# Optimization experiments

Measured on AMD Instinct MI355X. Metric: run time of the kernel, lower is better.

The kernel has to match this reference:

```python
import jax, jax.numpy as jnp
import numpy as np

N = 100_000      # nodes
E = 3_200_000    # edges (avg degree 32)
IN = 128         # input feature dim
H1, C1 = 8, 8    # layer-1 heads, channels per head (concat -> 64)
OUT = 2          # output classes (layer-2: 1 head, mean/no-concat)
NEG = 0.2        # LeakyReLU negative slope (PyG default)


def setup_inputs() -> dict:
    key = jax.random.key(0)
    ks = jax.random.split(key, 11)
    s1 = 1.0 / np.sqrt(IN)
    s2 = 1.0 / np.sqrt(H1 * C1)
    return {
        "x": jax.random.normal(ks[0], (N, IN), jnp.float32),
        "edge_index": jax.random.randint(ks[1], (2, E), 0, N, dtype=jnp.int32),
        "edge_attr": jax.random.normal(ks[2], (E, 1), jnp.float32),
        "W1": jax.random.normal(ks[3], (IN, H1 * C1), jnp.float32) * s1,
        "a1_src": jax.random.normal(ks[4], (H1, C1), jnp.float32) * s1,
        "a1_dst": jax.random.normal(ks[5], (H1, C1), jnp.float32) * s1,
        "b1": jnp.zeros((H1 * C1,), jnp.float32),
        "W2": jax.random.normal(ks[6], (H1 * C1, OUT), jnp.float32) * s2,
        "a2_src": jax.random.normal(ks[7], (1, OUT), jnp.float32) * s2,
        "a2_dst": jax.random.normal(ks[8], (1, OUT), jnp.float32) * s2,
        "b2": jnp.zeros((OUT,), jnp.float32),
    }


def gat_conv(x, W, a_src, a_dst, b, src, dst, heads, ch, concat):
    """PyG GATConv: per-head linear, per-edge LeakyReLU attention, segment softmax over dst."""
    n = x.shape[0]
    h = (x @ W).reshape(n, heads, ch)                 # [N, H, C]
    al_src = jnp.sum(h * a_src, axis=-1)              # [N, H]
    al_dst = jnp.sum(h * a_dst, axis=-1)              # [N, H]
    e = al_src[src] + al_dst[dst]                     # [Etot, H]
    e = jnp.where(e > 0, e, NEG * e)                  # LeakyReLU
    m = jax.lax.stop_gradient(jax.ops.segment_max(e, dst, num_segments=n))
    ex = jnp.exp(e - m[dst])
    den = jax.ops.segment_sum(ex, dst, num_segments=n)
    alpha = ex / den[dst]                             # segment softmax
    out = jax.ops.segment_sum(alpha[:, :, None] * h[src], dst, num_segments=n)  # [N, H, C]
    out = out.reshape(n, heads * ch) if concat else out.mean(axis=1)
    return out + b


def reference(x, edge_index, edge_attr, W1, a1_src, a1_dst, b1, W2, a2_src, a2_dst, b2):
    # add_self_loops=True (PyG default)
    loops = jnp.arange(x.shape[0], dtype=edge_index.dtype)
    src = jnp.concatenate([edge_index[0], loops])
    dst = jnp.concatenate([edge_index[1], loops])
    h = gat_conv(x, W1, a1_src, a1_dst, b1, src, dst, H1, C1, True)
    h = jax.nn.elu(h)
    return gat_conv(h, W2, a2_src, a2_dst, b2, src, dst, 1, OUT, False)
```

## Files before the change

### kernel.cpp

```cpp
#include <hip/hip_runtime.h>
#include <math.h>

#define NNODES 100000
#define NEDGES 3200000
#define ETOT   (NEDGES + NNODES)
#define IN_DIM 128
#define NH1    8
#define NC1    8
#define HC     64
#define OUTC   2
#define NEGSL  0.2f
#define L2E    1.44269504f

#define NBUCK 391
#define EPB   4096
#define NBLK  782
#define TOTC  (NBUCK * NBLK)


__global__ __launch_bounds__(256) void histA(const int* __restrict__ ei,
                                             int* __restrict__ carr) {
    __shared__ int lh[NBUCK];
    int tid = threadIdx.x;
    for (int i = tid; i < NBUCK; i += 256) lh[i] = 0;
    __syncthreads();
    const int* dptr = ei + NEDGES;
    int base = blockIdx.x * EPB;
#pragma unroll
    for (int i = 0; i < EPB / 1024; i++) {
        int idx = base + i * 1024 + tid * 4;
        if (idx < NEDGES) {
            int4 d4 = *(const int4*)&dptr[idx];
            atomicAdd(&lh[d4.x >> 8], 1);
            atomicAdd(&lh[d4.y >> 8], 1);
            atomicAdd(&lh[d4.z >> 8], 1);
            atomicAdd(&lh[d4.w >> 8], 1);
        }
    }
    __syncthreads();
    for (int i = tid; i < NBUCK; i += 256)
        carr[i * NBLK + blockIdx.x] = lh[i];
}

__global__ __launch_bounds__(256) void scanA(int* __restrict__ carr,
                                             int* __restrict__ bsums) {
    int gid = blockIdx.x * 256 + threadIdx.x;
    int v = (gid < TOTC) ? carr[gid] : 0;
    int lane = threadIdx.x & 63, w = threadIdx.x >> 6;
    int x = v;
    for (int off = 1; off < 64; off <<= 1) {
        int y = __shfl_up(x, off, 64);
        if (lane >= off) x += y;
    }
    __shared__ int wt[4];
    if (lane == 63) wt[w] = x;
    __syncthreads();
    int add = 0;
    for (int i = 0; i < w; i++) add += wt[i];
    int incl = x + add;
    if (gid < TOTC) carr[gid] = incl - v;
    if (threadIdx.x == 255) bsums[blockIdx.x] = incl;
}

__global__ __launch_bounds__(1024) void scanB(int* __restrict__ bsums, int nb) {
    int tid = threadIdx.x;
    int base = tid * 4;
    int v[4]; int tot = 0;
#pragma unroll
    for (int j = 0; j < 4; j++) {
        v[j] = (base + j < nb) ? bsums[base + j] : 0;
        tot += v[j];
    }
    int lane = tid & 63, w = tid >> 6;
    int x = tot;
    for (int off = 1; off < 64; off <<= 1) {
        int y = __shfl_up(x, off, 64);
        if (lane >= off) x += y;
    }
    __shared__ int wt[16];
    if (lane == 63) wt[w] = x;
    __syncthreads();
    int add = 0;
    for (int i = 0; i < w; i++) add += wt[i];
    int pre = x + add - tot;
#pragma unroll
    for (int j = 0; j < 4; j++) {
        if (base + j < nb) bsums[base + j] = pre;
        pre += v[j];
    }
}

__global__ __launch_bounds__(256) void scanC(int* __restrict__ carr,
                                             const int* __restrict__ bsums) {
    int gid = blockIdx.x * 256 + threadIdx.x;
    if (gid < TOTC) carr[gid] += bsums[gid >> 8];
}

__global__ __launch_bounds__(256) void scatC(const int* __restrict__ ei,
                                             const int* __restrict__ soff,
                                             int* __restrict__ ebuf) {
    __shared__ int soffL[NBUCK];
    __shared__ int lh[NBUCK];
    int tid = threadIdx.x;
    for (int i = tid; i < NBUCK; i += 256) {
        soffL[i] = soff[i * NBLK + blockIdx.x];
        lh[i] = 0;
    }
    __syncthreads();
    int base = blockIdx.x * EPB;
#pragma unroll
    for (int i = 0; i < EPB / 1024; i++) {
        int idx = base + i * 1024 + tid * 4;
        if (idx < NEDGES) {
            int4 s4 = *(const int4*)&ei[idx];
            int4 d4 = *(const int4*)&ei[NEDGES + idx];
            int b0 = d4.x >> 8, b1 = d4.y >> 8, b2 = d4.z >> 8, b3 = d4.w >> 8;
            int r0 = atomicAdd(&lh[b0], 1);
            int r1 = atomicAdd(&lh[b1], 1);
            int r2 = atomicAdd(&lh[b2], 1);
            int r3 = atomicAdd(&lh[b3], 1);
            ebuf[soffL[b0] + r0] = s4.x | ((d4.x & 255) << 17);
            ebuf[soffL[b1] + r1] = s4.y | ((d4.y & 255) << 17);
            ebuf[soffL[b2] + r2] = s4.z | ((d4.z & 255) << 17);
            ebuf[soffL[b3] + r3] = s4.w | ((d4.w & 255) << 17);
        }
    }
}

__global__ __launch_bounds__(256) void buildD(const int* __restrict__ soff,
                                              const int* __restrict__ ebuf,
                                              int* __restrict__ rowoff,
                                              int* __restrict__ srcs) {
    int b = blockIdx.x, tid = threadIdx.x;
    int nb = min(256, NNODES - b * 256);
    int ebeg = soff[b * NBLK];
    int eend = (b == NBUCK - 1) ? NEDGES : soff[(b + 1) * NBLK];
    __shared__ int cnt2[256];
    __shared__ int rowL[256];
    __shared__ int wsum[4];
    cnt2[tid] = 0;
    __syncthreads();
    for (int e = ebeg + tid; e < eend; e += 256)
        atomicAdd(&cnt2[(ebuf[e] >> 17) & 255], 1);
    __syncthreads();
    int v = (tid < nb) ? cnt2[tid] + 1 : 0;
    int lane = tid & 63, w = tid >> 6;
    int x = v;
    for (int off = 1; off < 64; off <<= 1) {
        int y = __shfl_up(x, off, 64);
        if (lane >= off) x += y;
    }
    if (lane == 63) wsum[w] = x;
    __syncthreads();
    int add = 0;
    for (int i = 0; i < w; i++) add += wsum[i];
    int fbase = ebeg + b * 256;
    int row = fbase + x + add - v;
    if (tid < nb) {
        rowL[tid] = row;
        int gnode = b * 256 + tid;
        rowoff[gnode] = row;
        srcs[row + cnt2[tid]] = gnode;
        if (gnode == NNODES - 1) rowoff[NNODES] = ETOT;
    }
    __syncthreads();
    cnt2[tid] = 0;
    __syncthreads();
    for (int e = ebeg + tid; e < eend; e += 256) {
        int wv = ebuf[e];
        int dl = (wv >> 17) & 255;
        int r = atomicAdd(&cnt2[dl], 1);
        srcs[rowL[dl] + r] = wv & 0x1FFFF;
    }
}


__global__ __launch_bounds__(256) void gemm1(const float* __restrict__ x,
                                             const float* __restrict__ W1,
                                             const float* __restrict__ a1s,
                                             const float* __restrict__ a1d,
                                             unsigned short* __restrict__ h1b,
                                             float2* __restrict__ alE,
                                             float* __restrict__ al1d) {
    __shared__ float sW[IN_DIM * HC];
    int tid = threadIdx.x;
    const float4* W4 = (const float4*)W1;
    float4* sW4 = (float4*)sW;
#pragma unroll
    for (int i = 0; i < 8; i++)
        sW4[tid + i * 256] = W4[tid + i * 256];
    __syncthreads();

    int w = __builtin_amdgcn_readfirstlane(tid >> 6);
    int lane = tid & 63;
    int node0 = blockIdx.x * 16 + w * 4;
    const float* xr = x + (size_t)node0 * IN_DIM;

    float acc0 = 0.f, acc1 = 0.f, acc2 = 0.f, acc3 = 0.f;
#pragma unroll 8
    for (int k = 0; k < IN_DIM; k++) {
        float wv = sW[k * HC + lane];
        acc0 = fmaf(xr[k], wv, acc0);
        acc1 = fmaf(xr[IN_DIM + k], wv, acc1);
        acc2 = fmaf(xr[2 * IN_DIM + k], wv, acc2);
        acc3 = fmaf(xr[3 * IN_DIM + k], wv, acc3);
    }

    float accs[4] = {acc0, acc1, acc2, acc3};
    int head = lane >> 3, c = lane & 7;
    float as = a1s[head * NC1 + c], adv = a1d[head * NC1 + c];
#pragma unroll
    for (int n = 0; n < 4; n++) {
        int node = node0 + n;
        unsigned int u = __float_as_uint(accs[n]);
        h1b[node * HC + lane] =
            (unsigned short)((u + 0x7FFF + ((u >> 16) & 1)) >> 16);
        float ps = accs[n] * as;
        float pd = accs[n] * adv;
        for (int off = 1; off < 8; off <<= 1) {
            ps += __shfl_xor(ps, off, 64);
            pd += __shfl_xor(pd, off, 64);
        }
        if (c == 0) {
            alE[node * NH1 + head] = make_float2(exp2f(ps * L2E),
                                                 exp2f(ps * (NEGSL * L2E)));
            al1d[node * NH1 + head] = pd;
        }
    }
}


__global__ __launch_bounds__(256) void agg1(const unsigned short* __restrict__ h1b,
                                            const float2* __restrict__ alE,
                                            const float* __restrict__ al1d,
                                            const float* __restrict__ b1,
                                            const float* __restrict__ W2,
                                            const float* __restrict__ a2s,
                                            const float* __restrict__ a2d,
                                            const int* __restrict__ rowoff,
                                            const int* __restrict__ srcs,
                                            float4* __restrict__ nd2,
                                            float* __restrict__ al2d) {
    int w = threadIdx.x >> 6, lane = threadIdx.x & 63;
    int node = blockIdx.x * 4 + w;
    if (node >= NNODES) return;
    int ep = lane >> 5;
    int c  = lane & 31;
    int hh = c >> 2;
    float ald = al1d[node * NH1 + hh];
    float E1d = exp2f(ald * L2E);
    float E2d = exp2f(ald * (NEGSL * L2E));
    int beg = __builtin_amdgcn_readfirstlane(rowoff[node]);
    int end = __builtin_amdgcn_readfirstlane(rowoff[node + 1]);

    float den = 0.f, acc0 = 0.f, acc1 = 0.f;
    float denB = 0.f, acc0B = 0.f, acc1B = 0.f;
    int i = beg;
    for (; i + 4 <= end; i += 4) {
        int sa = srcs[i + ep];
        int sb = srcs[i + 2 + ep];
        float2 ea = alE[sa * NH1 + hh];
        float2 eb = alE[sb * NH1 + hh];
        unsigned int ha = *(const unsigned int*)&h1b[sa * HC + 2 * c];
        unsigned int hb = *(const unsigned int*)&h1b[sb * HC + 2 * c];
        float pa = fmaxf(ea.x * E1d, ea.y * E2d);
        float pb = fmaxf(eb.x * E1d, eb.y * E2d);
        float va0 = __uint_as_float(ha << 16);
        float va1 = __uint_as_float(ha & 0xFFFF0000u);
        float vb0 = __uint_as_float(hb << 16);
        float vb1 = __uint_as_float(hb & 0xFFFF0000u);
        den  += pa;  acc0  = fmaf(pa, va0, acc0);  acc1  = fmaf(pa, va1, acc1);
        denB += pb;  acc0B = fmaf(pb, vb0, acc0B); acc1B = fmaf(pb, vb1, acc1B);
    }
    for (; i < end; i += 2) {
        int ia = i + ep;
        bool valid = ia < end;
        int sa = srcs[valid ? ia : end - 1];
        float2 ea = alE[sa * NH1 + hh];
        unsigned int ha = *(const unsigned int*)&h1b[sa * HC + 2 * c];
        float pa = fmaxf(ea.x * E1d, ea.y * E2d);
        pa = valid ? pa : 0.f;
        float va0 = __uint_as_float(ha << 16);
        float va1 = __uint_as_float(ha & 0xFFFF0000u);
        den += pa; acc0 = fmaf(pa, va0, acc0); acc1 = fmaf(pa, va1, acc1);
    }
    den += denB; acc0 += acc0B; acc1 += acc1B;
    den  += __shfl_xor(den, 32, 64);
    acc0 += __shfl_xor(acc0, 32, 64);
    acc1 += __shfl_xor(acc1, 32, 64);

    float2 b1v = *(const float2*)&b1[2 * c];
    float o0 = acc0 / den + b1v.x;
    float o1 = acc1 / den + b1v.y;
    o0 = (o0 > 0.f) ? o0 : expm1f(o0);
    o1 = (o1 > 0.f) ? o1 : expm1f(o1);
    float4 w2v = *(const float4*)&W2[4 * c];
    float p0 = o0 * w2v.x + o1 * w2v.z;
    float p1 = o0 * w2v.y + o1 * w2v.w;
    for (int off = 1; off < 32; off <<= 1) {
        p0 += __shfl_xor(p0, off, 64);
        p1 += __shfl_xor(p1, off, 64);
    }
    if (lane == 0) {
        float l2s = p0 * a2s[0] + p1 * a2s[1];
        float l2d = p0 * a2d[0] + p1 * a2d[1];
        nd2[node] = make_float4(exp2f(l2s * L2E), exp2f(l2s * (NEGSL * L2E)),
                                p0, p1);
        al2d[node] = l2d;
    }
}


__global__ __launch_bounds__(256) void agg2(const float4* __restrict__ nd2,
                                            const float* __restrict__ al2d,
                                            const float* __restrict__ b2,
                                            const int* __restrict__ rowoff,
                                            const int* __restrict__ srcs,
                                            float* __restrict__ out) {
    int w = threadIdx.x >> 6, lane = threadIdx.x & 63;
    int n = blockIdx.x * 4 + w;
    if (n >= NNODES) return;
    float ald = al2d[n];
    float E1d = exp2f(ald * L2E);
    float E2d = exp2f(ald * (NEGSL * L2E));
    int beg = rowoff[n], end = rowoff[n + 1];
    float den = 0.f, a0 = 0.f, a1 = 0.f;
    for (int idx = beg + lane; idx < end; idx += 64) {
        int s = srcs[idx];
        float4 nd = nd2[s];
        float p = fmaxf(nd.x * E1d, nd.y * E2d);
        den += p;
        a0 = fmaf(p, nd.z, a0);
        a1 = fmaf(p, nd.w, a1);
    }
    for (int off = 1; off < 64; off <<= 1) {
        den += __shfl_xor(den, off, 64);
        a0  += __shfl_xor(a0, off, 64);
        a1  += __shfl_xor(a1, off, 64);
    }
    if (lane == 0) {
        out[n * 2 + 0] = a0 / den + b2[0];
        out[n * 2 + 1] = a1 / den + b2[1];
    }
}


extern "C" void kernel_launch(void* const* d_in, const int* in_sizes, int n_in,
                              void* d_out, int out_size, void* d_ws, size_t ws_size,
                              hipStream_t stream) {
    const float* x   = (const float*)d_in[0];
    const int*   ei  = (const int*)  d_in[1];
    const float* W1  = (const float*)d_in[3];
    const float* a1s = (const float*)d_in[4];
    const float* a1d = (const float*)d_in[5];
    const float* b1  = (const float*)d_in[6];
    const float* W2  = (const float*)d_in[7];
    const float* a2s = (const float*)d_in[8];
    const float* a2d = (const float*)d_in[9];
    const float* b2  = (const float*)d_in[10];
    float* out = (float*)d_out;

    char* ws = (char*)d_ws;
    unsigned short* h1b = (unsigned short*)ws;
    float2* alE   = (float2*)(ws + (size_t)NNODES * HC * 2);
    float* al1d_  = (float*)(alE + (size_t)NNODES * NH1);
    float4* nd2   = (float4*)(al1d_ + (size_t)NNODES * NH1);
    float* al2d_  = (float*)(nd2 + NNODES);
    int* rowoff   = (int*)(al2d_ + NNODES);
    int* srcs     = rowoff + NNODES + 1;
    int* ebuf     = (int*)ws;
    int* carr     = ebuf + NEDGES;
    int* bsums    = carr + TOTC;

    const int NB_SC  = (TOTC + 255) / 256;
    const int NB_N4  = (NNODES + 3) / 4;
    const int NB_G   = NNODES / 16;

    histA<<<NBLK, 256, 0, stream>>>(ei, carr);
    scanA<<<NB_SC, 256, 0, stream>>>(carr, bsums);
    scanB<<<1, 1024, 0, stream>>>(bsums, NB_SC);
    scanC<<<NB_SC, 256, 0, stream>>>(carr, bsums);
    scatC<<<NBLK, 256, 0, stream>>>(ei, carr, ebuf);
    buildD<<<NBUCK, 256, 0, stream>>>(carr, ebuf, rowoff, srcs);

    gemm1<<<NB_G, 256, 0, stream>>>(x, W1, a1s, a1d, h1b, alE, al1d_);

    agg1<<<NB_N4, 256, 0, stream>>>(h1b, alE, al1d_, b1, W2, a2s, a2d,
                                    rowoff, srcs, nd2, al2d_);

    agg2<<<NB_N4, 256, 0, stream>>>(nd2, al2d_, b2, rowoff, srcs, out);
}
```

Measured before the change: 268.9 us.

## Fold scan fixup into consumers, widen CSR-build blocks, double gemm1 rows per wave

The scanC kernel is removed and its block-sum addition is folded into the reads in scatC and buildD. That saves one launch and one full read-write pass over the count array. histA, scatC and buildD now use 512-thread blocks, and buildD guards its per-node scan with tid<256. gemm1 now has each wave compute 8 nodes instead of 4, so each shared-memory W load is reused more and fewer blocks each reload W, at the cost of more registers per thread.

```diff
diff --git a/kernel.cpp b/kernel.cpp
--- a/kernel.cpp
+++ b/kernel.cpp
@@ -18,17 +18,17 @@
 #define TOTC  (NBUCK * NBLK)
 
 
-__global__ __launch_bounds__(256) void histA(const int* __restrict__ ei,
+__global__ __launch_bounds__(512) void histA(const int* __restrict__ ei,
                                              int* __restrict__ carr) {
     __shared__ int lh[NBUCK];
     int tid = threadIdx.x;
-    for (int i = tid; i < NBUCK; i += 256) lh[i] = 0;
+    for (int i = tid; i < NBUCK; i += 512) lh[i] = 0;
     __syncthreads();
     const int* dptr = ei + NEDGES;
     int base = blockIdx.x * EPB;
 #pragma unroll
-    for (int i = 0; i < EPB / 1024; i++) {
-        int idx = base + i * 1024 + tid * 4;
+    for (int i = 0; i < EPB / 2048; i++) {
+        int idx = base + i * 2048 + tid * 4;
         if (idx < NEDGES) {
             int4 d4 = *(const int4*)&dptr[idx];
             atomicAdd(&lh[d4.x >> 8], 1);
@@ -38,7 +38,7 @@
         }
     }
     __syncthreads();
-    for (int i = tid; i < NBUCK; i += 256)
+    for (int i = tid; i < NBUCK; i += 512)
         carr[i * NBLK + blockIdx.x] = lh[i];
 }
 
@@ -90,27 +90,23 @@
     }
 }
 
-__global__ __launch_bounds__(256) void scanC(int* __restrict__ carr,
-                                             const int* __restrict__ bsums) {
-    int gid = blockIdx.x * 256 + threadIdx.x;
-    if (gid < TOTC) carr[gid] += bsums[gid >> 8];
-}
-
-__global__ __launch_bounds__(256) void scatC(const int* __restrict__ ei,
-                                             const int* __restrict__ soff,
+__global__ __launch_bounds__(512) void scatC(const int* __restrict__ ei,
+                                             const int* __restrict__ carr,
+                                             const int* __restrict__ bsums,
                                              int* __restrict__ ebuf) {
     __shared__ int soffL[NBUCK];
     __shared__ int lh[NBUCK];
     int tid = threadIdx.x;
-    for (int i = tid; i < NBUCK; i += 256) {
-        soffL[i] = soff[i * NBLK + blockIdx.x];
+    for (int i = tid; i < NBUCK; i += 512) {
+        int g = i * NBLK + blockIdx.x;
+        soffL[i] = carr[g] + bsums[g >> 8];
         lh[i] = 0;
     }
     __syncthreads();
     int base = blockIdx.x * EPB;
 #pragma unroll
-    for (int i = 0; i < EPB / 1024; i++) {
-        int idx = base + i * 1024 + tid * 4;
+    for (int i = 0; i < EPB / 2048; i++) {
+        int idx = base + i * 2048 + tid * 4;
         if (idx < NEDGES) {
             int4 s4 = *(const int4*)&ei[idx];
             int4 d4 = *(const int4*)&ei[NEDGES + idx];
@@ -127,46 +123,53 @@
     }
 }
 
-__global__ __launch_bounds__(256) void buildD(const int* __restrict__ soff,
+__global__ __launch_bounds__(512) void buildD(const int* __restrict__ carr,
+                                              const int* __restrict__ bsums,
                                               const int* __restrict__ ebuf,
                                               int* __restrict__ rowoff,
                                               int* __restrict__ srcs) {
     int b = blockIdx.x, tid = threadIdx.x;
     int nb = min(256, NNODES - b * 256);
-    int ebeg = soff[b * NBLK];
-    int eend = (b == NBUCK - 1) ? NEDGES : soff[(b + 1) * NBLK];
+    int g0 = b * NBLK;
+    int ebeg = carr[g0] + bsums[g0 >> 8];
+    int eend = (b == NBUCK - 1) ? NEDGES
+                                : (carr[g0 + NBLK] + bsums[(g0 + NBLK) >> 8]);
     __shared__ int cnt2[256];
     __shared__ int rowL[256];
     __shared__ int wsum[4];
-    cnt2[tid] = 0;
-    __syncthreads();
-    for (int e = ebeg + tid; e < eend; e += 256)
+    if (tid < 256) cnt2[tid] = 0;
+    __syncthreads();
+    for (int e = ebeg + tid; e < eend; e += 512)
         atomicAdd(&cnt2[(ebuf[e] >> 17) & 255], 1);
     __syncthreads();
-    int v = (tid < nb) ? cnt2[tid] + 1 : 0;
-    int lane = tid & 63, w = tid >> 6;
-    int x = v;
-    for (int off = 1; off < 64; off <<= 1) {
-        int y = __shfl_up(x, off, 64);
-        if (lane >= off) x += y;
-    }
-    if (lane == 63) wsum[w] = x;
-    __syncthreads();
-    int add = 0;
-    for (int i = 0; i < w; i++) add += wsum[i];
-    int fbase = ebeg + b * 256;
-    int row = fbase + x + add - v;
-    if (tid < nb) {
-        rowL[tid] = row;
-        int gnode = b * 256 + tid;
-        rowoff[gnode] = row;
-        srcs[row + cnt2[tid]] = gnode;
-        if (gnode == NNODES - 1) rowoff[NNODES] = ETOT;
-    }
-    __syncthreads();
-    cnt2[tid] = 0;
-    __syncthreads();
-    for (int e = ebeg + tid; e < eend; e += 256) {
+    int lane = tid & 63, w4 = tid >> 6;
+    int v = 0, x = 0;
+    if (tid < 256) {
+        v = (tid < nb) ? cnt2[tid] + 1 : 0;
+        x = v;
+        for (int off = 1; off < 64; off <<= 1) {
+            int y = __shfl_up(x, off, 64);
+            if (lane >= off) x += y;
+        }
+        if (lane == 63) wsum[w4] = x;
+    }
+    __syncthreads();
+    if (tid < 256) {
+        int add = 0;
+        for (int i = 0; i < w4; i++) add += wsum[i];
+        int row = ebeg + b * 256 + x + add - v;
+        if (tid < nb) {
+            rowL[tid] = row;
+            int gnode = b * 256 + tid;
+            rowoff[gnode] = row;
+            srcs[row + cnt2[tid]] = gnode;
+            if (gnode == NNODES - 1) rowoff[NNODES] = ETOT;
+        }
+    }
+    __syncthreads();
+    if (tid < 256) cnt2[tid] = 0;
+    __syncthreads();
+    for (int e = ebeg + tid; e < eend; e += 512) {
         int wv = ebuf[e];
         int dl = (wv >> 17) & 255;
         int r = atomicAdd(&cnt2[dl], 1);
@@ -193,30 +196,28 @@
 
     int w = __builtin_amdgcn_readfirstlane(tid >> 6);
     int lane = tid & 63;
-    int node0 = blockIdx.x * 16 + w * 4;
+    int node0 = blockIdx.x * 32 + w * 8;
     const float* xr = x + (size_t)node0 * IN_DIM;
 
-    float acc0 = 0.f, acc1 = 0.f, acc2 = 0.f, acc3 = 0.f;
-#pragma unroll 8
+    float acc[8] = {0.f, 0.f, 0.f, 0.f, 0.f, 0.f, 0.f, 0.f};
+#pragma unroll 4
     for (int k = 0; k < IN_DIM; k++) {
         float wv = sW[k * HC + lane];
-        acc0 = fmaf(xr[k], wv, acc0);
-        acc1 = fmaf(xr[IN_DIM + k], wv, acc1);
-        acc2 = fmaf(xr[2 * IN_DIM + k], wv, acc2);
-        acc3 = fmaf(xr[3 * IN_DIM + k], wv, acc3);
-    }
-
-    float accs[4] = {acc0, acc1, acc2, acc3};
+#pragma unroll
+        for (int j = 0; j < 8; j++)
+            acc[j] = fmaf(xr[j * IN_DIM + k], wv, acc[j]);
+    }
+
     int head = lane >> 3, c = lane & 7;
     float as = a1s[head * NC1 + c], adv = a1d[head * NC1 + c];
 #pragma unroll
-    for (int n = 0; n < 4; n++) {
+    for (int n = 0; n < 8; n++) {
         int node = node0 + n;
-        unsigned int u = __float_as_uint(accs[n]);
+        unsigned int u = __float_as_uint(acc[n]);
         h1b[node * HC + lane] =
             (unsigned short)((u + 0x7FFF + ((u >> 16) & 1)) >> 16);
-        float ps = accs[n] * as;
-        float pd = accs[n] * adv;
+        float ps = acc[n] * as;
+        float pd = acc[n] * adv;
         for (int off = 1; off < 8; off <<= 1) {
             ps += __shfl_xor(ps, off, 64);
             pd += __shfl_xor(pd, off, 64);
@@ -374,14 +375,13 @@
 
     const int NB_SC  = (TOTC + 255) / 256;
     const int NB_N4  = (NNODES + 3) / 4;
-    const int NB_G   = NNODES / 16;
-
-    histA<<<NBLK, 256, 0, stream>>>(ei, carr);
+    const int NB_G   = NNODES / 32;
+
+    histA<<<NBLK, 512, 0, stream>>>(ei, carr);
     scanA<<<NB_SC, 256, 0, stream>>>(carr, bsums);
     scanB<<<1, 1024, 0, stream>>>(bsums, NB_SC);
-    scanC<<<NB_SC, 256, 0, stream>>>(carr, bsums);
-    scatC<<<NBLK, 256, 0, stream>>>(ei, carr, ebuf);
-    buildD<<<NBUCK, 256, 0, stream>>>(carr, ebuf, rowoff, srcs);
+    scatC<<<NBLK, 512, 0, stream>>>(ei, carr, bsums, ebuf);
+    buildD<<<NBUCK, 512, 0, stream>>>(carr, bsums, ebuf, rowoff, srcs);
 
     gemm1<<<NB_G, 256, 0, stream>>>(x, W1, a1s, a1d, h1b, alE, al1d_);
 
```

Result: slower. 277.2 us (+3.1%).
